# Performance work log

Measured on AMD Instinct MI355X. Metric: run time of the kernel, lower is better.

Reference implementation:

```python
import jax, jax.numpy as jnp
import numpy as np

LEAKY_SLOPE = 0.2  # tf.nn.leaky_relu default alpha


def _gat_layer(x, src, dst, W, a, n_nodes):
    # x: [N, F], W: [H, F, D], a: [H, 2D] (attention_fc weight, split into src/dst halves)
    H, F, D = W.shape
    z = jnp.einsum('nf,hfd->nhd', x, W)                    # [N, H, D] per-head projection
    a_s, a_d = a[:, :D], a[:, D:]
    # attn_fc(concat(z_src, z_dst)) == z_src @ a[:D] + z_dst @ a[D:]
    es = jnp.einsum('nhd,hd->nh', z, a_s)                  # [N, H]
    ed = jnp.einsum('nhd,hd->nh', z, a_d)                  # [N, H]
    e = jax.nn.leaky_relu(es[src] + ed[dst], negative_slope=LEAKY_SLOPE)  # [E, H]
    # segment softmax over each destination node's incoming edges
    m = jax.ops.segment_max(e, dst, num_segments=n_nodes)  # [N, H]
    ex = jnp.exp(e - m[dst])                               # [E, H]
    denom = jax.ops.segment_sum(ex, dst, num_segments=n_nodes)  # [N, H]
    alpha = ex / denom[dst]                                # [E, H]
    h = jax.ops.segment_sum(alpha[:, :, None] * z[src], dst, num_segments=n_nodes)  # [N, H, D]
    return h.reshape(n_nodes, H * D)                       # 'cat' merge over heads


def setup_inputs() -> dict:
    key = jax.random.key(0)
    k = jax.random.split(key, 8)
    N, E, F = 50000, 800000, 128
    D1, H1 = 32, 4
    D2, H2 = 32, 1
    features = jax.random.normal(k[0], (N, F), dtype=jnp.float32)
    src = jax.random.randint(k[1], (E,), 0, N, dtype=jnp.int32)
    dst = jax.random.randint(k[2], (E,), 0, N, dtype=jnp.int32)
    s1 = 1.0 / np.sqrt(F)
    s2 = 1.0 / np.sqrt(H1 * D1)
    W1 = jax.random.normal(k[3], (H1, F, D1), dtype=jnp.float32) * s1
    a1 = jax.random.normal(k[4], (H1, 2 * D1), dtype=jnp.float32) * (1.0 / np.sqrt(2 * D1))
    W2 = jax.random.normal(k[5], (H2, H1 * D1, D2), dtype=jnp.float32) * s2
    a2 = jax.random.normal(k[6], (H2, 2 * D2), dtype=jnp.float32) * (1.0 / np.sqrt(2 * D2))
    return {"features": features, "W1": W1, "a1": a1, "W2": W2, "a2": a2, "src": src, "dst": dst}


def reference(features, W1, a1, W2, a2, src, dst):
    n_nodes = features.shape[0]
    # NOTE: the original GATLayer stores `activation` but never applies it in call();
    # layers are pure attention aggregations, faithful to the source code.
    h = _gat_layer(features, src, dst, W1, a1, n_nodes)  # layer 1: 4 heads, cat -> [N, 128]
    out = _gat_layer(h, src, dst, W2, a2, n_nodes)       # layer 2: 1 head -> [N, 32] logits
    return out
```

## Files before the change

kernel.cpp:

```cpp
#include <hip/hip_runtime.h>
#include <hip/hip_bf16.h>

#define LEAKY 0.2f
#define SCAN_CHUNK 1024
#define BSH 6
#define NBMAX 1024
#define SORTB 256

typedef __attribute__((ext_vector_type(2))) _Float16 half2v;
typedef __attribute__((ext_vector_type(8))) _Float16 half8v;

#if __has_builtin(__builtin_amdgcn_fdot2)
__device__ __forceinline__ float fdot2(half2v a, half2v b, float c) {
    return __builtin_amdgcn_fdot2(a, b, c, false);
}
#else
__device__ __forceinline__ float fdot2(half2v a, half2v b, float c) {
    return c + (float)a[0] * (float)b[0] + (float)a[1] * (float)b[1];
}
#endif

__device__ __forceinline__ unsigned short bf16bits(float f) {
    __hip_bfloat16 h = __float2bfloat16(f);
    return *reinterpret_cast<unsigned short*>(&h);
}
__device__ __forceinline__ float bf16val(unsigned short u) {
    unsigned v = (unsigned)u << 16;
    return __uint_as_float(v);
}


__global__ __launch_bounds__(256) void hist_blk(const int* __restrict__ dst,
                                                int* __restrict__ hist,
                                                int E, int NB, int CPB) {
    __shared__ int h[NBMAX];
    const int blk = blockIdx.x, t = threadIdx.x;
    for (int i = t; i < NB; i += 256) h[i] = 0;
    __syncthreads();
    const int e0 = blk * CPB, e1 = min(e0 + CPB, E);
    for (int e = e0 + t; e < e1; e += 256) atomicAdd(&h[dst[e] >> BSH], 1);
    __syncthreads();
    int* __restrict__ hr = hist + (size_t)blk * NB;
    for (int i = t; i < NB; i += 256) hr[i] = h[i];
}

__global__ __launch_bounds__(256) void col_scan(int* __restrict__ hist,
                                                int* __restrict__ bcur,
                                                int NB, int B) {
    const int lane = threadIdx.x & 63;
    const int b = (blockIdx.x * blockDim.x + threadIdx.x) >> 6;
    if (b >= NB) return;
    int run = 0;
    for (int base = 0; base < B; base += 64) {
        const int blk = base + lane;
        const int v = (blk < B) ? hist[(size_t)blk * NB + b] : 0;
        int s = v;
        #pragma unroll
        for (int off = 1; off < 64; off <<= 1) {
            int x = __shfl_up(s, off);
            if (lane >= off) s += x;
        }
        if (blk < B) hist[(size_t)blk * NB + b] = run + s - v;
        run += __shfl(s, 63);
    }
    if (lane == 0) bcur[b] = run;
}

__global__ __launch_bounds__(256) void place_blk(const int* __restrict__ src,
                                                 const int* __restrict__ dst,
                                                 const int* __restrict__ hist,
                                                 uint2* __restrict__ ebuf,
                                                 int E, int NB, int CPB, int CAP) {
    __shared__ int cur[NBMAX];
    const int blk = blockIdx.x, t = threadIdx.x;
    const int* __restrict__ hr = hist + (size_t)blk * NB;
    for (int i = t; i < NB; i += 256) cur[i] = hr[i];
    __syncthreads();
    const int e0 = blk * CPB, e1 = min(e0 + CPB, E);
    for (int e = e0 + t; e < e1; e += 256) {
        const int d = dst[e];
        const int b = d >> BSH;
        int pos = atomicAdd(&cur[b], 1);
        if (pos >= CAP) pos = CAP - 1;
        ebuf[(size_t)b * CAP + pos] = make_uint2((unsigned)src[e], (unsigned)d);
    }
}

__global__ __launch_bounds__(256) void bucket_count(const uint2* __restrict__ ebuf,
                                                    const int* __restrict__ bcur,
                                                    int* __restrict__ cnt, int N, int CAP) {
    __shared__ int h[64];
    const int b  = blockIdx.x;
    const int n0 = b << BSH;
    const int t  = threadIdx.x;
    if (t < 64) h[t] = 0;
    __syncthreads();
    const int ne = min(bcur[b], CAP);
    const uint2* __restrict__ eb = ebuf + (size_t)b * CAP;
    for (int i = t; i < ne; i += 256) {
        atomicAdd(&h[(int)eb[i].y & 63], 1);
    }
    __syncthreads();
    if (t < 64 && n0 + t < N) cnt[n0 + t] = h[t];
}

__global__ __launch_bounds__(256) void bucket_place(const uint2* __restrict__ ebuf,
                                                    const int* __restrict__ bcur,
                                                    const int* __restrict__ rowptr,
                                                    int* __restrict__ csrc, int N, int CAP) {
    __shared__ int r[64];
    __shared__ int base[64];
    const int b  = blockIdx.x;
    const int n0 = b << BSH;
    const int t  = threadIdx.x;
    if (t < 64) {
        r[t] = 0;
        base[t] = (n0 + t < N) ? rowptr[n0 + t] : 0;
    }
    __syncthreads();
    const int ne = min(bcur[b], CAP);
    const uint2* __restrict__ eb = ebuf + (size_t)b * CAP;
    for (int i = t; i < ne; i += 256) {
        uint2 ed_ = eb[i];
        int li = (int)ed_.y & 63;
        int rk = atomicAdd(&r[li], 1);
        csrc[base[li] + rk] = (int)ed_.x;
    }
}

__global__ __launch_bounds__(256) void scan1(const int* __restrict__ cnt, int* __restrict__ part,
                                             int* __restrict__ bsum, int n) {
    __shared__ int s[256];
    const int base = blockIdx.x * SCAN_CHUNK;
    const int t = threadIdx.x;
    int v[4], sum = 0;
    #pragma unroll
    for (int i = 0; i < 4; ++i) {
        int idx = base + t * 4 + i;
        v[i] = (idx < n) ? cnt[idx] : 0;
        sum += v[i];
    }
    s[t] = sum;
    __syncthreads();
    for (int off = 1; off < 256; off <<= 1) {
        int x = (t >= off) ? s[t - off] : 0;
        __syncthreads();
        s[t] += x;
        __syncthreads();
    }
    int excl = (t == 0) ? 0 : s[t - 1];
    if (t == 255) bsum[blockIdx.x] = s[255];
    #pragma unroll
    for (int i = 0; i < 4; ++i) {
        int idx = base + t * 4 + i;
        if (idx < n) part[idx] = excl;
        excl += v[i];
    }
}

__global__ __launch_bounds__(256) void scan2(int* __restrict__ bsum, int nb) {
    __shared__ int s[256];
    const int t = threadIdx.x;
    s[t] = (t < nb) ? bsum[t] : 0;
    __syncthreads();
    for (int off = 1; off < 256; off <<= 1) {
        int x = (t >= off) ? s[t - off] : 0;
        __syncthreads();
        s[t] += x;
        __syncthreads();
    }
    if (t < nb) bsum[t] = (t == 0) ? 0 : s[t - 1];
}

__global__ void scan3(const int* __restrict__ part, const int* __restrict__ bsum,
                      int* __restrict__ rowptr, int n, int E) {
    int i = blockIdx.x * blockDim.x + threadIdx.x;
    if (i < n) rowptr[i] = part[i] + bsum[i / SCAN_CHUNK];
    if (i == n) rowptr[n] = E;
}

template<int COLS>
__global__ __launch_bounds__(16 * COLS / 4) void gemm_t(
    const float* __restrict__ X, const float* __restrict__ W,
    float* __restrict__ Z, unsigned short* __restrict__ Zb, int N, int HD)
{
    constexpr int TC = COLS / 4;
    constexpr int NT = 16 * TC;
    __shared__ __align__(16) half2v XsT[64][68];
    __shared__ __align__(16) half2v Ws2[64][COLS];

    const int tid  = threadIdx.x;
    const int row0 = blockIdx.x * 64;
    const int col0 = blockIdx.y * COLS;

    for (int i = tid; i < 64 * 32; i += NT) {
        const int row = i >> 5, kq = i & 31;
        float4 xv = make_float4(0.f, 0.f, 0.f, 0.f);
        if (row0 + row < N) xv = *(const float4*)&X[(size_t)(row0 + row) * 128 + kq * 4];
        half2v a; a[0] = (_Float16)xv.x; a[1] = (_Float16)xv.y;
        half2v b; b[0] = (_Float16)xv.z; b[1] = (_Float16)xv.w;
        XsT[kq * 2][row]     = a;
        XsT[kq * 2 + 1][row] = b;
    }
    for (int i = tid; i < 64 * COLS; i += NT) {
        const int kp = i / COLS, c = i % COLS;
        const int hd = col0 + c;
        const size_t base = (size_t)(hd >> 5) * (128 * 32) + (hd & 31);
        half2v wv;
        wv[0] = (_Float16)W[base + (size_t)(2 * kp) * 32];
        wv[1] = (_Float16)W[base + (size_t)(2 * kp + 1) * 32];
        Ws2[kp][c] = wv;
    }
    __syncthreads();

    const int tr = tid / TC;
    const int tc = tid % TC;

    float acc[4][4] = {};
    #pragma unroll 4
    for (int kp = 0; kp < 64; ++kp) {
        half8v xv = *(const half8v*)&XsT[kp][tr * 4];
        half8v wv = *(const half8v*)&Ws2[kp][tc * 4];
        #pragma unroll
        for (int i = 0; i < 4; ++i) {
            half2v xi; xi[0] = xv[2 * i]; xi[1] = xv[2 * i + 1];
            #pragma unroll
            for (int j = 0; j < 4; ++j) {
                half2v wj; wj[0] = wv[2 * j]; wj[1] = wv[2 * j + 1];
                acc[i][j] = fdot2(xi, wj, acc[i][j]);
            }
        }
    }

    #pragma unroll
    for (int i = 0; i < 4; ++i) {
        const int row = row0 + tr * 4 + i;
        if (row < N) {
            float4 o = make_float4(acc[i][0], acc[i][1], acc[i][2], acc[i][3]);
            *(float4*)&Z[(size_t)row * HD + col0 + tc * 4] = o;
            ushort4 ub;
            ub.x = bf16bits(o.x); ub.y = bf16bits(o.y);
            ub.z = bf16bits(o.z); ub.w = bf16bits(o.w);
            *(ushort4*)&Zb[(size_t)row * HD + col0 + tc * 4] = ub;
        }
    }
}

__global__ void attn_coef(const float* __restrict__ Z, const float* __restrict__ a,
                          float* __restrict__ es, float* __restrict__ ed,
                          int NH, int H) {
    int i = blockIdx.x * blockDim.x + threadIdx.x;
    if (i >= NH) return;
    int h = i % H;
    const float* zp = Z + (size_t)i * 32;
    const float* as = a + (size_t)h * 64;
    const float* ad = as + 32;
    float s = 0.0f, d_ = 0.0f;
    #pragma unroll
    for (int d = 0; d < 32; d += 4) {
        float4 zv = *(const float4*)&zp[d];
        float4 av = *(const float4*)&as[d];
        float4 dv = *(const float4*)&ad[d];
        s  += zv.x * av.x + zv.y * av.y + zv.z * av.z + zv.w * av.w;
        d_ += zv.x * dv.x + zv.y * dv.y + zv.z * dv.z + zv.w * dv.w;
    }
    es[i] = s;
    ed[i] = d_;
}

__global__ __launch_bounds__(256) void gat_node4(
    const unsigned short* __restrict__ Zb, const float* __restrict__ es,
    const float* __restrict__ ed, const int* __restrict__ rowptr,
    const int* __restrict__ csrc, float* __restrict__ Hout, int N)
{
    const int lane = threadIdx.x & 63;
    const int node = (blockIdx.x * blockDim.x + threadIdx.x) >> 6;
    if (node >= N) return;

    const int half = lane >> 5;
    const int cl   = lane & 31;
    const int head = cl >> 3;
    const float edv = ed[node * 4 + head];
    const int beg = rowptr[node];
    const int deg = rowptr[node + 1] - beg;
    const int* __restrict__ cp = csrc + beg;

    float4 acc = make_float4(0.f, 0.f, 0.f, 0.f);
    float den = 0.f;

    int j = 0;
    for (; j + 4 <= deg; j += 4) {
        const int sA = cp[j + half];
        const int sB = cp[j + 2 + half];
        const float qA = es[(unsigned)sA * 4u + head];
        const float qB = es[(unsigned)sB * 4u + head];
        const ushort4 uA = *(const ushort4*)&Zb[(unsigned)sA * 128u + cl * 4];
        const ushort4 uB = *(const ushort4*)&Zb[(unsigned)sB * 128u + cl * 4];
        float eA = qA + edv; eA = fmaxf(eA, LEAKY * eA);
        float eB = qB + edv; eB = fmaxf(eB, LEAKY * eB);
        const float pA = __expf(eA), pB = __expf(eB);
        den += pA + pB;
        acc.x = fmaf(pA, bf16val(uA.x), acc.x);
        acc.y = fmaf(pA, bf16val(uA.y), acc.y);
        acc.z = fmaf(pA, bf16val(uA.z), acc.z);
        acc.w = fmaf(pA, bf16val(uA.w), acc.w);
        acc.x = fmaf(pB, bf16val(uB.x), acc.x);
        acc.y = fmaf(pB, bf16val(uB.y), acc.y);
        acc.z = fmaf(pB, bf16val(uB.z), acc.z);
        acc.w = fmaf(pB, bf16val(uB.w), acc.w);
    }
    {
        const int ja = j + half;
        if (ja < deg) {
            const int s = cp[ja];
            const float q = es[(unsigned)s * 4u + head];
            const ushort4 u = *(const ushort4*)&Zb[(unsigned)s * 128u + cl * 4];
            float e = q + edv; e = fmaxf(e, LEAKY * e);
            const float p = __expf(e);
            den += p;
            acc.x = fmaf(p, bf16val(u.x), acc.x);
            acc.y = fmaf(p, bf16val(u.y), acc.y);
            acc.z = fmaf(p, bf16val(u.z), acc.z);
            acc.w = fmaf(p, bf16val(u.w), acc.w);
        }
        const int jb = j + 2 + half;
        if (jb < deg) {
            const int s = cp[jb];
            const float q = es[(unsigned)s * 4u + head];
            const ushort4 u = *(const ushort4*)&Zb[(unsigned)s * 128u + cl * 4];
            float e = q + edv; e = fmaxf(e, LEAKY * e);
            const float p = __expf(e);
            den += p;
            acc.x = fmaf(p, bf16val(u.x), acc.x);
            acc.y = fmaf(p, bf16val(u.y), acc.y);
            acc.z = fmaf(p, bf16val(u.z), acc.z);
            acc.w = fmaf(p, bf16val(u.w), acc.w);
        }
    }

    den   += __shfl_xor(den, 32);
    acc.x += __shfl_xor(acc.x, 32);
    acc.y += __shfl_xor(acc.y, 32);
    acc.z += __shfl_xor(acc.z, 32);
    acc.w += __shfl_xor(acc.w, 32);

    if (half == 0) {
        float4 o;
        if (deg > 0) {
            const float r = 1.0f / den;
            o = make_float4(acc.x * r, acc.y * r, acc.z * r, acc.w * r);
        } else {
            o = make_float4(0.f, 0.f, 0.f, 0.f);
        }
        *(float4*)&Hout[(size_t)node * 128 + cl * 4] = o;
    }
}

__global__ __launch_bounds__(256) void gat_node1(
    const unsigned short* __restrict__ Zb, const float* __restrict__ es,
    const float* __restrict__ ed, const int* __restrict__ rowptr,
    const int* __restrict__ csrc, float* __restrict__ Hout, int N)
{
    const int lane = threadIdx.x & 63;
    const int node = (blockIdx.x * blockDim.x + threadIdx.x) >> 6;
    if (node >= N) return;

    const int grp = lane >> 3;
    const int cl  = lane & 7;
    const float edv = ed[node];
    const int beg = rowptr[node];
    const int deg = rowptr[node + 1] - beg;
    const int* __restrict__ cp = csrc + beg;

    float4 acc = make_float4(0.f, 0.f, 0.f, 0.f);
    float den = 0.f;

    int j = 0;
    for (; j + 8 <= deg; j += 8) {
        const int s = cp[j + grp];
        const float q = es[s];
        const ushort4 u = *(const ushort4*)&Zb[(unsigned)s * 32u + cl * 4];
        float e = q + edv; e = fmaxf(e, LEAKY * e);
        const float p = __expf(e);
        den += p;
        acc.x = fmaf(p, bf16val(u.x), acc.x);
        acc.y = fmaf(p, bf16val(u.y), acc.y);
        acc.z = fmaf(p, bf16val(u.z), acc.z);
        acc.w = fmaf(p, bf16val(u.w), acc.w);
    }
    {
        const int jt = j + grp;
        if (jt < deg) {
            const int s = cp[jt];
            const float q = es[s];
            const ushort4 u = *(const ushort4*)&Zb[(unsigned)s * 32u + cl * 4];
            float e = q + edv; e = fmaxf(e, LEAKY * e);
            const float p = __expf(e);
            den += p;
            acc.x = fmaf(p, bf16val(u.x), acc.x);
            acc.y = fmaf(p, bf16val(u.y), acc.y);
            acc.z = fmaf(p, bf16val(u.z), acc.z);
            acc.w = fmaf(p, bf16val(u.w), acc.w);
        }
    }

    #pragma unroll
    for (int off = 8; off < 64; off <<= 1) {
        den   += __shfl_xor(den, off);
        acc.x += __shfl_xor(acc.x, off);
        acc.y += __shfl_xor(acc.y, off);
        acc.z += __shfl_xor(acc.z, off);
        acc.w += __shfl_xor(acc.w, off);
    }

    if (grp == 0) {
        float4 o;
        if (deg > 0) {
            const float r = 1.0f / den;
            o = make_float4(acc.x * r, acc.y * r, acc.z * r, acc.w * r);
        } else {
            o = make_float4(0.f, 0.f, 0.f, 0.f);
        }
        *(float4*)&Hout[(size_t)node * 32 + cl * 4] = o;
    }
}

extern "C" void kernel_launch(void* const* d_in, const int* in_sizes, int n_in,
                              void* d_out, int out_size, void* d_ws, size_t ws_size,
                              hipStream_t stream) {
    const float* features = (const float*)d_in[0];
    const float* W1 = (const float*)d_in[1];
    const float* a1 = (const float*)d_in[2];
    const float* W2 = (const float*)d_in[3];
    const float* a2 = (const float*)d_in[4];
    const int*   src = (const int*)d_in[5];
    const int*   dst = (const int*)d_in[6];
    float* out = (float*)d_out;

    const int N  = in_sizes[0] / 128;
    const int E  = in_sizes[5];
    const int H1 = in_sizes[2] / 64;

    const int NB  = (N + 63) >> BSH;
    const int CAP = (((E / NB) * 3 / 2) + 255) & ~255;
    const int CPB = (E + SORTB - 1) / SORTB;

    char* wsb = (char*)d_ws;
    size_t ob = 0;
    auto alloc_b = [&](size_t bytes) {
        ob = (ob + 15) & ~(size_t)15;
        char* p = wsb + ob; ob += bytes; return p;
    };

    int* cnt    = (int*)alloc_b((size_t)N * 4);
    int* bcur   = (int*)alloc_b((size_t)NB * 4);
    int* hist   = (int*)alloc_b((size_t)SORTB * NB * 4);
    int* part   = (int*)alloc_b((size_t)N * 4);
    int* bsum   = (int*)alloc_b(256 * 4);
    int* rowptr = (int*)alloc_b((size_t)(N + 1) * 4);
    int* csrc   = (int*)alloc_b((size_t)E * 4);
    float* z1   = (float*)alloc_b((size_t)N * 128 * 4);
    float* h1   = (float*)alloc_b((size_t)N * 128 * 4);
    float* es1  = (float*)alloc_b((size_t)N * H1 * 4);
    float* ed1  = (float*)alloc_b((size_t)N * H1 * 4);
    float* z2   = (float*)alloc_b((size_t)N * 32 * 4);
    float* es2  = (float*)alloc_b((size_t)N * 4);
    float* ed2  = (float*)alloc_b((size_t)N * 4);
    unsigned short* zb1 = (unsigned short*)alloc_b((size_t)N * 128 * 2);
    unsigned short* zb2 = (unsigned short*)alloc_b((size_t)N * 32 * 2);

    uint2* ebuf = (uint2*)z1;

    const int B = 256;
    #define GRID(n) (((n) + B - 1) / B)
    const int nb = (N + SCAN_CHUNK - 1) / SCAN_CHUNK;

    hist_blk<<<SORTB, 256, 0, stream>>>(dst, hist, E, NB, CPB);
    col_scan<<<GRID(NB * 64), 256, 0, stream>>>(hist, bcur, NB, SORTB);
    place_blk<<<SORTB, 256, 0, stream>>>(src, dst, hist, ebuf, E, NB, CPB, CAP);
    bucket_count<<<NB, 256, 0, stream>>>(ebuf, bcur, cnt, N, CAP);
    scan1<<<nb, B, 0, stream>>>(cnt, part, bsum, N);
    scan2<<<1, B, 0, stream>>>(bsum, nb);
    scan3<<<GRID(N + 1), B, 0, stream>>>(part, bsum, rowptr, N, E);
    bucket_place<<<NB, 256, 0, stream>>>(ebuf, bcur, rowptr, csrc, N, CAP);

    const int RB = (N + 63) / 64;

    gemm_t<64><<<dim3(RB, 2), 256, 0, stream>>>(features, W1, z1, zb1, N, 128);
    attn_coef<<<GRID(N * H1), B, 0, stream>>>(z1, a1, es1, ed1, N * H1, H1);
    gat_node4<<<GRID(N * 64), B, 0, stream>>>(zb1, es1, ed1, rowptr, csrc, h1, N);

    gemm_t<32><<<dim3(RB, 1), 128, 0, stream>>>(h1, W2, z2, zb2, N, 32);
    attn_coef<<<GRID(N), B, 0, stream>>>(z2, a2, es2, ed2, N, 1);
    gat_node1<<<GRID(N * 64), B, 0, stream>>>(zb2, es2, ed2, rowptr, csrc, out, N);

    #undef GRID
    (void)n_in; (void)out_size; (void)ws_size;
}
```

Before: 248.8 us.

## Fuse attention coefficient computation into GEMM epilogue and unroll edge aggregation loops

Result: faster. 228.0 us (-8.4%).

```diff
diff --git a/kernel.cpp b/kernel.cpp
--- a/kernel.cpp
+++ b/kernel.cpp
@@ -182,7 +182,8 @@
 template<int COLS>
 __global__ __launch_bounds__(16 * COLS / 4) void gemm_t(
     const float* __restrict__ X, const float* __restrict__ W,
-    float* __restrict__ Z, unsigned short* __restrict__ Zb, int N, int HD)
+    const float* __restrict__ Aat, unsigned short* __restrict__ Zb,
+    float* __restrict__ es, float* __restrict__ ed, int N, int HD, int H)
 {
     constexpr int TC = COLS / 4;
     constexpr int NT = 16 * TC;
@@ -236,37 +237,45 @@
     for (int i = 0; i < 4; ++i) {
         const int row = row0 + tr * 4 + i;
         if (row < N) {
-            float4 o = make_float4(acc[i][0], acc[i][1], acc[i][2], acc[i][3]);
-            *(float4*)&Z[(size_t)row * HD + col0 + tc * 4] = o;
             ushort4 ub;
-            ub.x = bf16bits(o.x); ub.y = bf16bits(o.y);
-            ub.z = bf16bits(o.z); ub.w = bf16bits(o.w);
+            ub.x = bf16bits(acc[i][0]); ub.y = bf16bits(acc[i][1]);
+            ub.z = bf16bits(acc[i][2]); ub.w = bf16bits(acc[i][3]);
             *(ushort4*)&Zb[(size_t)row * HD + col0 + tc * 4] = ub;
         }
     }
-}
-
-__global__ void attn_coef(const float* __restrict__ Z, const float* __restrict__ a,
-                          float* __restrict__ es, float* __restrict__ ed,
-                          int NH, int H) {
-    int i = blockIdx.x * blockDim.x + threadIdx.x;
-    if (i >= NH) return;
-    int h = i % H;
-    const float* zp = Z + (size_t)i * 32;
-    const float* as = a + (size_t)h * 64;
-    const float* ad = as + 32;
-    float s = 0.0f, d_ = 0.0f;
+
+    const int hg = (col0 + tc * 4) >> 5;
+    const int cw = (tc & 7) * 4;
+    const float4 as4 = *(const float4*)&Aat[(size_t)hg * 64 + cw];
+    const float4 ad4 = *(const float4*)&Aat[(size_t)hg * 64 + 32 + cw];
     #pragma unroll
-    for (int d = 0; d < 32; d += 4) {
-        float4 zv = *(const float4*)&zp[d];
-        float4 av = *(const float4*)&as[d];
-        float4 dv = *(const float4*)&ad[d];
-        s  += zv.x * av.x + zv.y * av.y + zv.z * av.z + zv.w * av.w;
-        d_ += zv.x * dv.x + zv.y * dv.y + zv.z * dv.z + zv.w * dv.w;
-    }
-    es[i] = s;
-    ed[i] = d_;
-}
+    for (int i = 0; i < 4; ++i) {
+        float se = acc[i][0] * as4.x + acc[i][1] * as4.y + acc[i][2] * as4.z + acc[i][3] * as4.w;
+        float de = acc[i][0] * ad4.x + acc[i][1] * ad4.y + acc[i][2] * ad4.z + acc[i][3] * ad4.w;
+        se += __shfl_xor(se, 1); de += __shfl_xor(de, 1);
+        se += __shfl_xor(se, 2); de += __shfl_xor(de, 2);
+        se += __shfl_xor(se, 4); de += __shfl_xor(de, 4);
+        const int row = row0 + tr * 4 + i;
+        if ((tc & 7) == 0 && row < N) {
+            es[(size_t)row * H + hg] = se;
+            ed[(size_t)row * H + hg] = de;
+        }
+    }
+}
+
+#define EDGE4(sE)                                                              \
+    {                                                                          \
+        const int s_ = (sE);                                                   \
+        const float q_ = es[(unsigned)s_ * 4u + head];                         \
+        const ushort4 u_ = *(const ushort4*)&Zb[(unsigned)s_ * 128u + cl * 4]; \
+        float e_ = q_ + edv; e_ = fmaxf(e_, LEAKY * e_);                       \
+        const float p_ = __expf(e_);                                           \
+        den += p_;                                                             \
+        acc.x = fmaf(p_, bf16val(u_.x), acc.x);                                \
+        acc.y = fmaf(p_, bf16val(u_.y), acc.y);                                \
+        acc.z = fmaf(p_, bf16val(u_.z), acc.z);                                \
+        acc.w = fmaf(p_, bf16val(u_.w), acc.w);                                \
+    }
 
 __global__ __launch_bounds__(256) void gat_node4(
     const unsigned short* __restrict__ Zb, const float* __restrict__ es,
@@ -289,13 +298,104 @@
     float den = 0.f;
 
     int j = 0;
-    for (; j + 4 <= deg; j += 4) {
-        const int sA = cp[j + half];
-        const int sB = cp[j + 2 + half];
-        const float qA = es[(unsigned)sA * 4u + head];
-        const float qB = es[(unsigned)sB * 4u + head];
-        const ushort4 uA = *(const ushort4*)&Zb[(unsigned)sA * 128u + cl * 4];
-        const ushort4 uB = *(const ushort4*)&Zb[(unsigned)sB * 128u + cl * 4];
+    for (; j + 8 <= deg; j += 8) {
+        const int s0 = cp[j + half];
+        const int s1 = cp[j + 2 + half];
+        const int s2 = cp[j + 4 + half];
+        const int s3 = cp[j + 6 + half];
+        const float q0 = es[(unsigned)s0 * 4u + head];
+        const float q1 = es[(unsigned)s1 * 4u + head];
+        const float q2 = es[(unsigned)s2 * 4u + head];
+        const float q3 = es[(unsigned)s3 * 4u + head];
+        const ushort4 u0 = *(const ushort4*)&Zb[(unsigned)s0 * 128u + cl * 4];
+        const ushort4 u1 = *(const ushort4*)&Zb[(unsigned)s1 * 128u + cl * 4];
+        const ushort4 u2 = *(const ushort4*)&Zb[(unsigned)s2 * 128u + cl * 4];
+        const ushort4 u3 = *(const ushort4*)&Zb[(unsigned)s3 * 128u + cl * 4];
+        float e0 = q0 + edv; e0 = fmaxf(e0, LEAKY * e0);
+        float e1 = q1 + edv; e1 = fmaxf(e1, LEAKY * e1);
+        float e2 = q2 + edv; e2 = fmaxf(e2, LEAKY * e2);
+        float e3 = q3 + edv; e3 = fmaxf(e3, LEAKY * e3);
+        const float p0 = __expf(e0), p1 = __expf(e1);
+        const float p2 = __expf(e2), p3 = __expf(e3);
+        den += p0 + p1 + p2 + p3;
+        acc.x = fmaf(p0, bf16val(u0.x), acc.x);
+        acc.y = fmaf(p0, bf16val(u0.y), acc.y);
+        acc.z = fmaf(p0, bf16val(u0.z), acc.z);
+        acc.w = fmaf(p0, bf16val(u0.w), acc.w);
+        acc.x = fmaf(p1, bf16val(u1.x), acc.x);
+        acc.y = fmaf(p1, bf16val(u1.y), acc.y);
+        acc.z = fmaf(p1, bf16val(u1.z), acc.z);
+        acc.w = fmaf(p1, bf16val(u1.w), acc.w);
+        acc.x = fmaf(p2, bf16val(u2.x), acc.x);
+        acc.y = fmaf(p2, bf16val(u2.y), acc.y);
+        acc.z = fmaf(p2, bf16val(u2.z), acc.z);
+        acc.w = fmaf(p2, bf16val(u2.w), acc.w);
+        acc.x = fmaf(p3, bf16val(u3.x), acc.x);
+        acc.y = fmaf(p3, bf16val(u3.y), acc.y);
+        acc.z = fmaf(p3, bf16val(u3.z), acc.z);
+        acc.w = fmaf(p3, bf16val(u3.w), acc.w);
+    }
+    for (; j + 2 <= deg; j += 2) EDGE4(cp[j + half]);
+    if (j < deg && half == 0)   EDGE4(cp[j]);
+
+    den   += __shfl_xor(den, 32);
+    acc.x += __shfl_xor(acc.x, 32);
+    acc.y += __shfl_xor(acc.y, 32);
+    acc.z += __shfl_xor(acc.z, 32);
+    acc.w += __shfl_xor(acc.w, 32);
+
+    if (half == 0) {
+        float4 o;
+        if (deg > 0) {
+            const float r = 1.0f / den;
+            o = make_float4(acc.x * r, acc.y * r, acc.z * r, acc.w * r);
+        } else {
+            o = make_float4(0.f, 0.f, 0.f, 0.f);
+        }
+        *(float4*)&Hout[(size_t)node * 128 + cl * 4] = o;
+    }
+}
+
+#define EDGE1(sE)                                                             \
+    {                                                                         \
+        const int s_ = (sE);                                                  \
+        const float q_ = es[s_];                                              \
+        const ushort4 u_ = *(const ushort4*)&Zb[(unsigned)s_ * 32u + cl * 4]; \
+        float e_ = q_ + edv; e_ = fmaxf(e_, LEAKY * e_);                      \
+        const float p_ = __expf(e_);                                          \
+        den += p_;                                                            \
+        acc.x = fmaf(p_, bf16val(u_.x), acc.x);                               \
+        acc.y = fmaf(p_, bf16val(u_.y), acc.y);                               \
+        acc.z = fmaf(p_, bf16val(u_.z), acc.z);                               \
+        acc.w = fmaf(p_, bf16val(u_.w), acc.w);                               \
+    }
+
+__global__ __launch_bounds__(256) void gat_node1(
+    const unsigned short* __restrict__ Zb, const float* __restrict__ es,
+    const float* __restrict__ ed, const int* __restrict__ rowptr,
+    const int* __restrict__ csrc, float* __restrict__ Hout, int N)
+{
+    const int lane = threadIdx.x & 63;
+    const int node = (blockIdx.x * blockDim.x + threadIdx.x) >> 6;
+    if (node >= N) return;
+
+    const int grp = lane >> 3;
+    const int cl  = lane & 7;
+    const float edv = ed[node];
+    const int beg = rowptr[node];
+    const int deg = rowptr[node + 1] - beg;
+    const int* __restrict__ cp = csrc + beg;
+
+    float4 acc = make_float4(0.f, 0.f, 0.f, 0.f);
+    float den = 0.f;
+
+    int j = 0;
+    for (; j + 16 <= deg; j += 16) {
+        const int sA = cp[j + grp];
+        const int sB = cp[j + 8 + grp];
+        const float qA = es[sA], qB = es[sB];
+        const ushort4 uA = *(const ushort4*)&Zb[(unsigned)sA * 32u + cl * 4];
+        const ushort4 uB = *(const ushort4*)&Zb[(unsigned)sB * 32u + cl * 4];
         float eA = qA + edv; eA = fmaxf(eA, LEAKY * eA);
         float eB = qB + edv; eB = fmaxf(eB, LEAKY * eB);
         const float pA = __expf(eA), pB = __expf(eB);
@@ -309,100 +409,8 @@
         acc.z = fmaf(pB, bf16val(uB.z), acc.z);
         acc.w = fmaf(pB, bf16val(uB.w), acc.w);
     }
-    {
-        const int ja = j + half;
-        if (ja < deg) {
-            const int s = cp[ja];
-            const float q = es[(unsigned)s * 4u + head];
-            const ushort4 u = *(const ushort4*)&Zb[(unsigned)s * 128u + cl * 4];
-            float e = q + edv; e = fmaxf(e, LEAKY * e);
-            const float p = __expf(e);
-            den += p;
-            acc.x = fmaf(p, bf16val(u.x), acc.x);
-            acc.y = fmaf(p, bf16val(u.y), acc.y);
-            acc.z = fmaf(p, bf16val(u.z), acc.z);
-            acc.w = fmaf(p, bf16val(u.w), acc.w);
-        }
-        const int jb = j + 2 + half;
-        if (jb < deg) {
-            const int s = cp[jb];
-            const float q = es[(unsigned)s * 4u + head];
-            const ushort4 u = *(const ushort4*)&Zb[(unsigned)s * 128u + cl * 4];
-            float e = q + edv; e = fmaxf(e, LEAKY * e);
-            const float p = __expf(e);
-            den += p;
-            acc.x = fmaf(p, bf16val(u.x), acc.x);
-            acc.y = fmaf(p, bf16val(u.y), acc.y);
-            acc.z = fmaf(p, bf16val(u.z), acc.z);
-            acc.w = fmaf(p, bf16val(u.w), acc.w);
-        }
-    }
-
-    den   += __shfl_xor(den, 32);
-    acc.x += __shfl_xor(acc.x, 32);
-    acc.y += __shfl_xor(acc.y, 32);
-    acc.z += __shfl_xor(acc.z, 32);
-    acc.w += __shfl_xor(acc.w, 32);
-
-    if (half == 0) {
-        float4 o;
-        if (deg > 0) {
-            const float r = 1.0f / den;
-            o = make_float4(acc.x * r, acc.y * r, acc.z * r, acc.w * r);
-        } else {
-            o = make_float4(0.f, 0.f, 0.f, 0.f);
-        }
-        *(float4*)&Hout[(size_t)node * 128 + cl * 4] = o;
-    }
-}
-
-__global__ __launch_bounds__(256) void gat_node1(
-    const unsigned short* __restrict__ Zb, const float* __restrict__ es,
-    const float* __restrict__ ed, const int* __restrict__ rowptr,
-    const int* __restrict__ csrc, float* __restrict__ Hout, int N)
-{
-    const int lane = threadIdx.x & 63;
-    const int node = (blockIdx.x * blockDim.x + threadIdx.x) >> 6;
-    if (node >= N) return;
-
-    const int grp = lane >> 3;
-    const int cl  = lane & 7;
-    const float edv = ed[node];
-    const int beg = rowptr[node];
-    const int deg = rowptr[node + 1] - beg;
-    const int* __restrict__ cp = csrc + beg;
-
-    float4 acc = make_float4(0.f, 0.f, 0.f, 0.f);
-    float den = 0.f;
-
-    int j = 0;
-    for (; j + 8 <= deg; j += 8) {
-        const int s = cp[j + grp];
-        const float q = es[s];
-        const ushort4 u = *(const ushort4*)&Zb[(unsigned)s * 32u + cl * 4];
-        float e = q + edv; e = fmaxf(e, LEAKY * e);
-        const float p = __expf(e);
-        den += p;
-        acc.x = fmaf(p, bf16val(u.x), acc.x);
-        acc.y = fmaf(p, bf16val(u.y), acc.y);
-        acc.z = fmaf(p, bf16val(u.z), acc.z);
-        acc.w = fmaf(p, bf16val(u.w), acc.w);
-    }
-    {
-        const int jt = j + grp;
-        if (jt < deg) {
-            const int s = cp[jt];
-            const float q = es[s];
-            const ushort4 u = *(const ushort4*)&Zb[(unsigned)s * 32u + cl * 4];
-            float e = q + edv; e = fmaxf(e, LEAKY * e);
-            const float p = __expf(e);
-            den += p;
-            acc.x = fmaf(p, bf16val(u.x), acc.x);
-            acc.y = fmaf(p, bf16val(u.y), acc.y);
-            acc.z = fmaf(p, bf16val(u.z), acc.z);
-            acc.w = fmaf(p, bf16val(u.w), acc.w);
-        }
-    }
+    for (; j + 8 <= deg; j += 8) EDGE1(cp[j + grp]);
+    if (j + grp < deg)           EDGE1(cp[j + grp]);
 
     #pragma unroll
     for (int off = 8; off < 64; off <<= 1) {
@@ -459,17 +467,14 @@
     int* bsum   = (int*)alloc_b(256 * 4);
     int* rowptr = (int*)alloc_b((size_t)(N + 1) * 4);
     int* csrc   = (int*)alloc_b((size_t)E * 4);
-    float* z1   = (float*)alloc_b((size_t)N * 128 * 4);
+    uint2* ebuf = (uint2*)alloc_b((size_t)NB * CAP * 8);
     float* h1   = (float*)alloc_b((size_t)N * 128 * 4);
     float* es1  = (float*)alloc_b((size_t)N * H1 * 4);
     float* ed1  = (float*)alloc_b((size_t)N * H1 * 4);
-    float* z2   = (float*)alloc_b((size_t)N * 32 * 4);
     float* es2  = (float*)alloc_b((size_t)N * 4);
     float* ed2  = (float*)alloc_b((size_t)N * 4);
     unsigned short* zb1 = (unsigned short*)alloc_b((size_t)N * 128 * 2);
     unsigned short* zb2 = (unsigned short*)alloc_b((size_t)N * 32 * 2);
-
-    uint2* ebuf = (uint2*)z1;
 
     const int B = 256;
     #define GRID(n) (((n) + B - 1) / B)
@@ -486,12 +491,10 @@
 
     const int RB = (N + 63) / 64;
 
-    gemm_t<64><<<dim3(RB, 2), 256, 0, stream>>>(features, W1, z1, zb1, N, 128);
-    attn_coef<<<GRID(N * H1), B, 0, stream>>>(z1, a1, es1, ed1, N * H1, H1);
+    gemm_t<64><<<dim3(RB, 2), 256, 0, stream>>>(features, W1, a1, zb1, es1, ed1, N, 128, 4);
     gat_node4<<<GRID(N * 64), B, 0, stream>>>(zb1, es1, ed1, rowptr, csrc, h1, N);
 
-    gemm_t<32><<<dim3(RB, 1), 128, 0, stream>>>(h1, W2, z2, zb2, N, 32);
-    attn_coef<<<GRID(N), B, 0, stream>>>(z2, a2, es2, ed2, N, 1);
+    gemm_t<32><<<dim3(RB, 1), 128, 0, stream>>>(h1, W2, a2, zb2, es2, ed2, N, 32, 1);
     gat_node1<<<GRID(N * 64), B, 0, stream>>>(zb2, es2, ed2, rowptr, csrc, out, N);
 
     #undef GRID
```
